# Kernel optimization log

Measured on AMD Instinct MI355X. Metric: run time of the kernel, lower is better.

## Reference

```python
import jax, jax.numpy as jnp
import numpy as np

B, G, D = 128, 1024, 128


def setup_inputs() -> dict:
    key = jax.random.key(0)
    k1, k2, k3 = jax.random.split(key, 3)
    h = jax.random.normal(k1, (B, G, D), dtype=jnp.float32)
    adj_c = jax.random.uniform(k2, (B, G, G), dtype=jnp.float32)
    phone_set = jax.random.randint(k3, (B,), 0, G, dtype=jnp.int64)
    return {"h": h, "adj_c": adj_c, "phone_set": phone_set}


def reference(h, adj_c, phone_set):
    # h: (B, G, D), adj_c: (B, G, G), phone_set: (B,) pivot indices
    B_, G_, D_ = h.shape
    p = phone_set.astype(jnp.int32)  # (B,)
    # Gather the pivot row of adj_c for each sample: adj_c[i, p_i, :]
    row = jnp.take_along_axis(adj_c, p[:, None, None], axis=1)[:, 0, :]  # (B, G)
    pos = jnp.arange(G_, dtype=jnp.int32)[None, :]  # (1, G)
    mask_bf = (pos < p[:, None]).astype(h.dtype)  # strictly before pivot
    mask_af = (pos > p[:, None]).astype(h.dtype)  # strictly after pivot
    # Masked weighted sums replace the per-sample (1,k)@(k,D) matmuls.
    # If phone == 0 (or phone == G-1) the mask is all-zero -> zeros(D),
    # matching the torch zeros(1, D) branch exactly.
    g_bf = jnp.einsum('bg,bgd->bd', row * mask_bf, h)  # (B, D)
    g_af = jnp.einsum('bg,bgd->bd', row * mask_af, h)  # (B, D)
    return g_bf, g_af
```

## Files before the change

kernel.cpp:

```cpp
#include <hip/hip_runtime.h>

constexpr int Bq = 128;
constexpr int Gq = 1024;
constexpr int Dq = 128;
constexpr int NDC = 8;

__global__ __launch_bounds__(512, 8) void agg_kernel(
    const float* __restrict__ h,
    const float* __restrict__ adj,
    const int*   __restrict__ phone,
    float*       __restrict__ out)
{
    const int b  = blockIdx.x;
    const int dc = blockIdx.y;
    const int t  = threadIdx.x;
    const int p  = phone[b];

    __shared__ float row_bf_s[Gq];
    __shared__ float row_af_s[Gq];
    if (t < 256) {
        const int j = t << 2;
        const float4 r = *reinterpret_cast<const float4*>(
            adj + ((long long)b * Gq + (long long)p) * Gq + j);
        float4 rb, ra;
        rb.x = (j + 0 < p) ? r.x : 0.0f;  ra.x = (j + 0 > p) ? r.x : 0.0f;
        rb.y = (j + 1 < p) ? r.y : 0.0f;  ra.y = (j + 1 > p) ? r.y : 0.0f;
        rb.z = (j + 2 < p) ? r.z : 0.0f;  ra.z = (j + 2 > p) ? r.z : 0.0f;
        rb.w = (j + 3 < p) ? r.w : 0.0f;  ra.w = (j + 3 > p) ? r.w : 0.0f;
        *reinterpret_cast<float4*>(row_bf_s + j) = rb;
        *reinterpret_cast<float4*>(row_af_s + j) = ra;
    }
    __syncthreads();

    const int dbase = dc * 16 + ((t & 3) << 2);
    const int rgrp  = t >> 2;
    const float* hb = h + (long long)b * Gq * Dq + dbase;

    float4 bf = make_float4(0.f, 0.f, 0.f, 0.f);
    float4 af = make_float4(0.f, 0.f, 0.f, 0.f);

    #pragma unroll 4
    for (int it = 0; it < Gq / 128; ++it) {
        const int g = rgrp + (it << 7);
        const float4 v = *reinterpret_cast<const float4*>(hb + g * Dq);
        const float wb = row_bf_s[g];
        const float wa = row_af_s[g];
        bf.x = fmaf(wb, v.x, bf.x);
        bf.y = fmaf(wb, v.y, bf.y);
        bf.z = fmaf(wb, v.z, bf.z);
        bf.w = fmaf(wb, v.w, bf.w);
        af.x = fmaf(wa, v.x, af.x);
        af.y = fmaf(wa, v.y, af.y);
        af.z = fmaf(wa, v.z, af.z);
        af.w = fmaf(wa, v.w, af.w);
    }

    #pragma unroll
    for (int m = 4; m <= 32; m <<= 1) {
        bf.x += __shfl_xor(bf.x, m, 64);
        bf.y += __shfl_xor(bf.y, m, 64);
        bf.z += __shfl_xor(bf.z, m, 64);
        bf.w += __shfl_xor(bf.w, m, 64);
        af.x += __shfl_xor(af.x, m, 64);
        af.y += __shfl_xor(af.y, m, 64);
        af.z += __shfl_xor(af.z, m, 64);
        af.w += __shfl_xor(af.w, m, 64);
    }

    __shared__ float4 pbf[8][4];
    __shared__ float4 paf[8][4];
    const int wave = t >> 6;
    const int lane = t & 63;
    if (lane < 4) {
        pbf[wave][lane] = bf;
        paf[wave][lane] = af;
    }
    __syncthreads();

    if (t < 4) {
        float4 sb = pbf[0][t];
        float4 sa = paf[0][t];
        #pragma unroll
        for (int wv = 1; wv < 8; ++wv) {
            const float4 ob = pbf[wv][t];
            const float4 oa = paf[wv][t];
            sb.x += ob.x; sb.y += ob.y; sb.z += ob.z; sb.w += ob.w;
            sa.x += oa.x; sa.y += oa.y; sa.z += oa.z; sa.w += oa.w;
        }
        const int d = dc * 16 + (t << 2);
        *reinterpret_cast<float4*>(out + b * Dq + d) = sb;
        *reinterpret_cast<float4*>(out + Bq * Dq + b * Dq + d) = sa;
    }
}

extern "C" void kernel_launch(void* const* d_in, const int* in_sizes, int n_in,
                              void* d_out, int out_size, void* d_ws, size_t ws_size,
                              hipStream_t stream) {
    const float* h     = (const float*)d_in[0];
    const float* adj   = (const float*)d_in[1];
    const int*   phone = (const int*)d_in[2];
    float* out = (float*)d_out;

    dim3 grid(Bq, NDC);
    agg_kernel<<<grid, 512, 0, stream>>>(h, adj, phone, out);
}
```

Measured before the change: 16.48 us.

## Preload all h rows and adjacency weights into registers, drop shared staging and barrier

Each thread now issues all eight float4 loads of h before reading phone and the pivot adjacency row. It then reads its eight weights straight from global memory and applies the before/after masks inline. This removes the shared-memory staging of the pivot row and the barrier that held up the h loads. More memory requests are in flight per thread, at the cost of more registers and of dropping the occupancy hint from launch bounds.

```diff
diff --git a/kernel.cpp b/kernel.cpp
--- a/kernel.cpp
+++ b/kernel.cpp
@@ -5,7 +5,7 @@
 constexpr int Dq = 128;
 constexpr int NDC = 8;
 
-__global__ __launch_bounds__(512, 8) void agg_kernel(
+__global__ __launch_bounds__(512) void agg_kernel(
     const float* __restrict__ h,
     const float* __restrict__ adj,
     const int*   __restrict__ phone,
@@ -14,45 +14,40 @@
     const int b  = blockIdx.x;
     const int dc = blockIdx.y;
     const int t  = threadIdx.x;
-    const int p  = phone[b];
-
-    __shared__ float row_bf_s[Gq];
-    __shared__ float row_af_s[Gq];
-    if (t < 256) {
-        const int j = t << 2;
-        const float4 r = *reinterpret_cast<const float4*>(
-            adj + ((long long)b * Gq + (long long)p) * Gq + j);
-        float4 rb, ra;
-        rb.x = (j + 0 < p) ? r.x : 0.0f;  ra.x = (j + 0 > p) ? r.x : 0.0f;
-        rb.y = (j + 1 < p) ? r.y : 0.0f;  ra.y = (j + 1 > p) ? r.y : 0.0f;
-        rb.z = (j + 2 < p) ? r.z : 0.0f;  ra.z = (j + 2 > p) ? r.z : 0.0f;
-        rb.w = (j + 3 < p) ? r.w : 0.0f;  ra.w = (j + 3 > p) ? r.w : 0.0f;
-        *reinterpret_cast<float4*>(row_bf_s + j) = rb;
-        *reinterpret_cast<float4*>(row_af_s + j) = ra;
-    }
-    __syncthreads();
 
     const int dbase = dc * 16 + ((t & 3) << 2);
     const int rgrp  = t >> 2;
     const float* hb = h + (long long)b * Gq * Dq + dbase;
 
+    float4 v[8];
+    #pragma unroll
+    for (int it = 0; it < 8; ++it) {
+        v[it] = *reinterpret_cast<const float4*>(hb + (rgrp + (it << 7)) * Dq);
+    }
+
+    const int p = phone[b];
+    const float* rowb = adj + ((long long)b * Gq + (long long)p) * Gq;
+    float w[8];
+    #pragma unroll
+    for (int it = 0; it < 8; ++it) {
+        w[it] = rowb[rgrp + (it << 7)];
+    }
+
     float4 bf = make_float4(0.f, 0.f, 0.f, 0.f);
     float4 af = make_float4(0.f, 0.f, 0.f, 0.f);
-
-    #pragma unroll 4
-    for (int it = 0; it < Gq / 128; ++it) {
+    #pragma unroll
+    for (int it = 0; it < 8; ++it) {
         const int g = rgrp + (it << 7);
-        const float4 v = *reinterpret_cast<const float4*>(hb + g * Dq);
-        const float wb = row_bf_s[g];
-        const float wa = row_af_s[g];
-        bf.x = fmaf(wb, v.x, bf.x);
-        bf.y = fmaf(wb, v.y, bf.y);
-        bf.z = fmaf(wb, v.z, bf.z);
-        bf.w = fmaf(wb, v.w, bf.w);
-        af.x = fmaf(wa, v.x, af.x);
-        af.y = fmaf(wa, v.y, af.y);
-        af.z = fmaf(wa, v.z, af.z);
-        af.w = fmaf(wa, v.w, af.w);
+        const float wb = (g < p) ? w[it] : 0.0f;
+        const float wa = (g > p) ? w[it] : 0.0f;
+        bf.x = fmaf(wb, v[it].x, bf.x);
+        bf.y = fmaf(wb, v[it].y, bf.y);
+        bf.z = fmaf(wb, v[it].z, bf.z);
+        bf.w = fmaf(wb, v[it].w, bf.w);
+        af.x = fmaf(wa, v[it].x, af.x);
+        af.y = fmaf(wa, v[it].y, af.y);
+        af.z = fmaf(wa, v[it].z, af.z);
+        af.w = fmaf(wa, v[it].w, af.w);
     }
 
     #pragma unroll
```

Result: no change. 16.41 us (-0.4%).
